# Optimization experiments

Measured on AMD Instinct MI355X. Metric: run time of the kernel, lower is better.

The kernel has to match this reference:

```python
import jax, jax.numpy as jnp
import numpy as np

MARGIN = 0.3


def _l2norm(x, axis=-1):
    return x / (jnp.linalg.norm(x, axis=axis, keepdims=True) + 1e-12)


def setup_inputs() -> dict:
    key = jax.random.key(0)
    k1, k2, k3, k4 = jax.random.split(key, 4)
    n, P, d = 1024, 8, 2048
    global_feat = jax.random.normal(k1, (n, d), dtype=jnp.float32)
    partial_feat = jax.random.normal(k2, (n, P, d), dtype=jnp.float32)
    part_labels = jax.random.randint(k3, (n, P), 0, 2).astype(jnp.float32)
    global_labels = jax.random.randint(k4, (n,), 0, 64).astype(jnp.int64)
    return {"global_feat": global_feat, "partial_feat": partial_feat,
            "part_labels": part_labels, "global_labels": global_labels}


def reference(global_feat, partial_feat, part_labels, global_labels):
    # --- compute_distance (VGTripletLoss) ---
    g = _l2norm(global_feat)            # [n, d]
    p = _l2norm(partial_feat)           # [n, P, d]
    gs = (1.0 - g @ g.T) / 2.0          # [n, n]
    overlap = part_labels[:, None, :] * part_labels[None, :, :]   # [n, n, P]
    # per-part cosine distance: [n, n, P]
    slf = (1.0 - jnp.einsum('ipd,jpd->ijp', p, p)) / 2.0
    slf = slf * overlap
    dist = (slf.sum(-1) + gs) / (overlap.sum(-1) + 1.0)            # [n, n]

    # --- compute_loss: hard positive/negative mining ---
    mask = global_labels[:, None] == global_labels[None, :]        # [n, n]
    neg_inf = jnp.float32(-1e30)
    pos_inf = jnp.float32(1e30)
    dist_ap = jnp.max(jnp.where(mask, dist, neg_inf), axis=1)      # hardest positive
    dist_an = jnp.min(jnp.where(mask, pos_inf, dist), axis=1)      # hardest negative
    # MarginRankingLoss(y=1, reduction='mean'): max(0, dist_ap - dist_an + margin)
    loss = jnp.mean(jax.nn.relu(dist_ap - dist_an + MARGIN))
    return loss
```

## Files before the change

### kernel.cpp

```cpp
#include <hip/hip_runtime.h>

#define N 1024
#define D 2048
#define P 8
#define F 9
#define KTOT (F * D)
#define BM 128
#define BKT 32
#define MARGIN 0.3f

typedef float f32x4 __attribute__((ext_vector_type(4)));
typedef short s16x8 __attribute__((ext_vector_type(8)));

#define GLOBAL_AS __attribute__((address_space(1)))
#define LDS_AS __attribute__((address_space(3)))

__device__ __forceinline__ const float* feat_row(const float* __restrict__ g,
                                                 const float* __restrict__ p,
                                                 int i, int f) {
    return (f == 0) ? (g + (size_t)i * D)
                    : (p + ((size_t)i * P + (f - 1)) * D);
}

__device__ __forceinline__ unsigned f2bf(float x) {
    unsigned u = __float_as_uint(x);
    return (u + 0x7fffu + ((u >> 16) & 1u)) >> 16;
}

__global__ __launch_bounds__(256)
void pack_kernel(const float* __restrict__ gfeat,
                 const float* __restrict__ pfeat,
                 const float* __restrict__ plab,
                 unsigned short* __restrict__ V) {
    const int wid = (blockIdx.x << 2) | (threadIdx.x >> 6);
    const int lane = threadIdx.x & 63;
    const int i = wid / F, f = wid % F;
    const float* src = feat_row(gfeat, pfeat, i, f);
    const float4* s4 = (const float4*)src;
    float4 a[4][2];
    #pragma unroll
    for (int q = 0; q < 4; ++q) {
        a[q][0] = s4[(q * 64 + lane) * 2];
        a[q][1] = s4[(q * 64 + lane) * 2 + 1];
    }
    float ss = 0.f;
    #pragma unroll
    for (int q = 0; q < 4; ++q)
        #pragma unroll
        for (int h = 0; h < 2; ++h)
            ss += a[q][h].x * a[q][h].x + a[q][h].y * a[q][h].y
                + a[q][h].z * a[q][h].z + a[q][h].w * a[q][h].w;
    #pragma unroll
    for (int m = 32; m > 0; m >>= 1) ss += __shfl_xor(ss, m, 64);
    const float ls = (f == 0) ? 1.0f : plab[i * P + (f - 1)];
    const float inv = ls / (sqrtf(ss) + 1e-12f);
    unsigned short* dst = V + (size_t)wid * D;
    #pragma unroll
    for (int q = 0; q < 4; ++q) {
        uint4 o;
        o.x = f2bf(a[q][0].x * inv) | (f2bf(a[q][0].y * inv) << 16);
        o.y = f2bf(a[q][0].z * inv) | (f2bf(a[q][0].w * inv) << 16);
        o.z = f2bf(a[q][1].x * inv) | (f2bf(a[q][1].y * inv) << 16);
        o.w = f2bf(a[q][1].z * inv) | (f2bf(a[q][1].w * inv) << 16);
        *(uint4*)&dst[(size_t)(q * 64 + lane) * 8] = o;
    }
}

__global__ __launch_bounds__(256)
void gemm_kernel(const unsigned short* __restrict__ V,
                 float* __restrict__ part, int ks) {
    __shared__ short As[2][BM * BKT];
    __shared__ short Bs[2][BM * BKT];

    const int nwg = gridDim.x * gridDim.y;
    const int l = blockIdx.x + gridDim.x * blockIdx.y;
    const int q = nwg >> 3;
    const int wg = (l & 7) * q + (l >> 3);
    const int t36 = wg % 36;
    const int bz = wg / 36;

    int by = 0, rem = t36;
    while (rem >= 8 - by) { rem -= 8 - by; ++by; }
    const int bx = by + rem;

    const int t = threadIdx.x;
    const int wave = t >> 6, lane = t & 63;
    const int i0 = by * BM;
    const int j0 = bx * BM;
    const int kbase = bz * ks;
    const int nsteps = ks >> 5;

    const int srow = t >> 2;
    const int schunk = (t & 3) ^ ((t >> 3) & 3);
    const unsigned short* Ag = V + (size_t)(i0 + srow) * KTOT + kbase + schunk * 8;
    const unsigned short* Bg = V + (size_t)(j0 + srow) * KTOT + kbase + schunk * 8;

    const int kq = lane >> 4;
    const int rsw = ((lane & 15) >> 1) & 3;
    const int kk = (kq ^ rsw) * 8;
    const int arow0 = (wave & 1) * 64 + (lane & 15);
    const int brow0 = (wave >> 1) * 64 + (lane & 15);

    f32x4 acc[4][4];
    #pragma unroll
    for (int m = 0; m < 4; ++m)
        #pragma unroll
        for (int n = 0; n < 4; ++n)
            acc[m][n] = (f32x4){0.f, 0.f, 0.f, 0.f};

#define STAGE(b) do {                                                          \
    __builtin_amdgcn_global_load_lds((const GLOBAL_AS void*)Ag,                \
        (LDS_AS void*)(&As[(b)][t * 8]), 16, 0, 0);                            \
    __builtin_amdgcn_global_load_lds((const GLOBAL_AS void*)(Ag + (size_t)64 * KTOT), \
        (LDS_AS void*)(&As[(b)][2048 + t * 8]), 16, 0, 0);                     \
    __builtin_amdgcn_global_load_lds((const GLOBAL_AS void*)Bg,                \
        (LDS_AS void*)(&Bs[(b)][t * 8]), 16, 0, 0);                            \
    __builtin_amdgcn_global_load_lds((const GLOBAL_AS void*)(Bg + (size_t)64 * KTOT), \
        (LDS_AS void*)(&Bs[(b)][2048 + t * 8]), 16, 0, 0);                     \
    Ag += BKT; Bg += BKT;                                                      \
} while (0)

#define COMPUTE(b) do {                                                        \
    s16x8 af[4], bf[4];                                                        \
    _Pragma("unroll")                                                          \
    for (int m = 0; m < 4; ++m)                                                \
        af[m] = *(const s16x8*)(&As[(b)][(arow0 + m * 16) * 32 + kk]);         \
    _Pragma("unroll")                                                          \
    for (int n = 0; n < 4; ++n)                                                \
        bf[n] = *(const s16x8*)(&Bs[(b)][(brow0 + n * 16) * 32 + kk]);         \
    _Pragma("unroll")                                                          \
    for (int m = 0; m < 4; ++m)                                                \
        _Pragma("unroll")                                                      \
        for (int n = 0; n < 4; ++n)                                            \
            acc[m][n] = __builtin_amdgcn_mfma_f32_16x16x32_bf16(               \
                af[m], bf[n], acc[m][n], 0, 0, 0);                             \
} while (0)

    STAGE(0);

    int cur = 0;
    for (int ksi = 0; ksi < nsteps - 1; ++ksi) {
        STAGE(cur ^ 1);
        asm volatile("s_waitcnt vmcnt(4)" ::: "memory");
        __builtin_amdgcn_s_barrier();
        COMPUTE(cur);
        __builtin_amdgcn_s_barrier();
        cur ^= 1;
    }
    asm volatile("s_waitcnt vmcnt(0)" ::: "memory");
    __builtin_amdgcn_s_barrier();
    COMPUTE(cur);

#undef STAGE
#undef COMPUTE

    float* outp = part + (size_t)bz * N * N;
    const int rbase = i0 + (wave & 1) * 64 + (lane >> 4) * 4;
    const int cbase = j0 + (wave >> 1) * 64 + (lane & 15);
    #pragma unroll
    for (int m = 0; m < 4; ++m)
        #pragma unroll
        for (int n = 0; n < 4; ++n)
            #pragma unroll
            for (int r = 0; r < 4; ++r)
                outp[(size_t)(rbase + m * 16 + r) * N + cbase + n * 16] = acc[m][n][r];

    if (bx != by) {
        #pragma unroll
        for (int m = 0; m < 4; ++m)
            #pragma unroll
            for (int n = 0; n < 4; ++n)
                #pragma unroll
                for (int r = 0; r < 4; ++r)
                    outp[(size_t)(cbase + n * 16) * N + rbase + m * 16 + r] = acc[m][n][r];
    }
}

template <int S>
__global__ __launch_bounds__(256)
void mine_kernel(const float* __restrict__ part,
                 const float* __restrict__ plab,
                 const int* __restrict__ glab,
                 float* __restrict__ rowloss) {
    const int i0 = blockIdx.x * 4;
    const int t = threadIdx.x;
    const int wave = t >> 6, lane = t & 63;
    const int j = t * 4;

    float labj[4][8];
    const float4* pj = (const float4*)&plab[(size_t)j * P];
    #pragma unroll
    for (int qq = 0; qq < 8; ++qq) ((float4*)labj)[qq] = pj[qq];
    const int4 gj = *(const int4*)&glab[j];
    const int gv[4] = {gj.x, gj.y, gj.z, gj.w};

    __shared__ float sap[4], san[4];

    #pragma unroll
    for (int ri = 0; ri < 4; ++ri) {
        const int i = i0 + ri;

        float4 dot = {0.f, 0.f, 0.f, 0.f};
        #pragma unroll
        for (int s = 0; s < S; ++s) {
            float4 v = *(const float4*)&part[(size_t)s * N * N + (size_t)i * N + j];
            dot.x += v.x; dot.y += v.y; dot.z += v.z; dot.w += v.w;
        }

        const int li = glab[i];
        float lab_i[P];
        #pragma unroll
        for (int c = 0; c < P; ++c) lab_i[c] = plab[i * P + c];

        float ap = -1e30f, an = 1e30f;
        const float dv[4] = {dot.x, dot.y, dot.z, dot.w};
        #pragma unroll
        for (int u = 0; u < 4; ++u) {
            float ov = 0.f;
            #pragma unroll
            for (int c = 0; c < P; ++c) ov += lab_i[c] * labj[u][c];
            float d = 0.5f - dv[u] / (2.0f * (ov + 1.0f));
            if (gv[u] == li) ap = fmaxf(ap, d);
            else             an = fminf(an, d);
        }

        #pragma unroll
        for (int m = 32; m > 0; m >>= 1) {
            ap = fmaxf(ap, __shfl_xor(ap, m, 64));
            an = fminf(an, __shfl_xor(an, m, 64));
        }
        if (lane == 0) { sap[wave] = ap; san[wave] = an; }
        __syncthreads();
        if (t == 0) {
            float A = fmaxf(fmaxf(sap[0], sap[1]), fmaxf(sap[2], sap[3]));
            float B = fminf(fminf(san[0], san[1]), fminf(san[2], san[3]));
            rowloss[i] = fmaxf(0.f, A - B + MARGIN);
        }
        __syncthreads();
    }
}

__global__ void reduce_kernel(const float* __restrict__ rowloss,
                              float* __restrict__ out) {
    const int t = threadIdx.x;
    float s = rowloss[t] + rowloss[t + 256] + rowloss[t + 512] + rowloss[t + 768];
    __shared__ float red[256];
    red[t] = s;
    __syncthreads();
    for (int st = 128; st > 0; st >>= 1) {
        if (t < st) red[t] += red[t + st];
        __syncthreads();
    }
    if (t == 0) out[0] = red[0] * (1.0f / N);
}

extern "C" void kernel_launch(void* const* d_in, const int* in_sizes, int n_in,
                              void* d_out, int out_size, void* d_ws, size_t ws_size,
                              hipStream_t stream) {
    const float* gfeat = (const float*)d_in[0];
    const float* pfeat = (const float*)d_in[1];
    const float* plab  = (const float*)d_in[2];
    const int*   glab  = (const int*)d_in[3];
    float* out = (float*)d_out;

    const size_t vbytes = (size_t)N * KTOT * 2;
    const size_t slice  = (size_t)N * N * 4;

    int S = (ws_size != 0 && ws_size >= vbytes + 16 * slice + 4096) ? 16 : 8;
    const int ks = KTOT / S;

    char* ws = (char*)d_ws;
    unsigned short* V = (unsigned short*)ws;
    float* part    = (float*)(ws + vbytes);
    float* rowloss = (float*)(ws + vbytes + (size_t)S * slice);

    pack_kernel<<<N * F / 4, 256, 0, stream>>>(gfeat, pfeat, plab, V);
    gemm_kernel<<<dim3(36, S), 256, 0, stream>>>(V, part, ks);
    if (S == 16)
        mine_kernel<16><<<N / 4, 256, 0, stream>>>(part, plab, glab, rowloss);
    else
        mine_kernel<8><<<N / 4, 256, 0, stream>>>(part, plab, glab, rowloss);
    reduce_kernel<<<1, 256, 0, stream>>>(rowloss, out);
}
```

Before: 164.1 us.

## Reduce split-K partial tiles with float atomics into one buffer

Split-K GEMM slices no longer write separate N×N partial buffers. They now atomically add into a single zeroed buffer, and the split count rises to 24. The mining kernel then reads one float4 per element instead of summing S slices, which removes most of the partial-buffer write and read traffic. The cost is atomic contention, an extra memset, and a summation order that is no longer deterministic.

```diff
diff --git a/kernel.cpp b/kernel.cpp
--- a/kernel.cpp
+++ b/kernel.cpp
@@ -7,6 +7,7 @@
 #define KTOT (F * D)
 #define BM 128
 #define BKT 32
+#define SPLIT 24
 #define MARGIN 0.3f
 
 typedef float f32x4 __attribute__((ext_vector_type(4)));
@@ -154,7 +155,6 @@
 #undef STAGE
 #undef COMPUTE
 
-    float* outp = part + (size_t)bz * N * N;
     const int rbase = i0 + (wave & 1) * 64 + (lane >> 4) * 4;
     const int cbase = j0 + (wave >> 1) * 64 + (lane & 15);
     #pragma unroll
@@ -163,7 +163,8 @@
         for (int n = 0; n < 4; ++n)
             #pragma unroll
             for (int r = 0; r < 4; ++r)
-                outp[(size_t)(rbase + m * 16 + r) * N + cbase + n * 16] = acc[m][n][r];
+                atomicAdd(&part[(size_t)(rbase + m * 16 + r) * N + cbase + n * 16],
+                          acc[m][n][r]);
 
     if (bx != by) {
         #pragma unroll
@@ -172,11 +173,11 @@
             for (int n = 0; n < 4; ++n)
                 #pragma unroll
                 for (int r = 0; r < 4; ++r)
-                    outp[(size_t)(cbase + n * 16) * N + rbase + m * 16 + r] = acc[m][n][r];
-    }
-}
-
-template <int S>
+                    atomicAdd(&part[(size_t)(cbase + n * 16) * N + rbase + m * 16 + r],
+                              acc[m][n][r]);
+    }
+}
+
 __global__ __launch_bounds__(256)
 void mine_kernel(const float* __restrict__ part,
                  const float* __restrict__ plab,
@@ -200,12 +201,7 @@
     for (int ri = 0; ri < 4; ++ri) {
         const int i = i0 + ri;
 
-        float4 dot = {0.f, 0.f, 0.f, 0.f};
-        #pragma unroll
-        for (int s = 0; s < S; ++s) {
-            float4 v = *(const float4*)&part[(size_t)s * N * N + (size_t)i * N + j];
-            dot.x += v.x; dot.y += v.y; dot.z += v.z; dot.w += v.w;
-        }
+        float4 dot = *(const float4*)&part[(size_t)i * N + j];
 
         const int li = glab[i];
         float lab_i[P];
@@ -264,21 +260,18 @@
     float* out = (float*)d_out;
 
     const size_t vbytes = (size_t)N * KTOT * 2;
-    const size_t slice  = (size_t)N * N * 4;
-
-    int S = (ws_size != 0 && ws_size >= vbytes + 16 * slice + 4096) ? 16 : 8;
-    const int ks = KTOT / S;
+    const size_t pbytes = (size_t)N * N * 4;
 
     char* ws = (char*)d_ws;
     unsigned short* V = (unsigned short*)ws;
     float* part    = (float*)(ws + vbytes);
-    float* rowloss = (float*)(ws + vbytes + (size_t)S * slice);
-
+    float* rowloss = (float*)(ws + vbytes + pbytes);
+
+    const int ks = KTOT / SPLIT;
+
+    hipMemsetAsync(part, 0, pbytes, stream);
     pack_kernel<<<N * F / 4, 256, 0, stream>>>(gfeat, pfeat, plab, V);
-    gemm_kernel<<<dim3(36, S), 256, 0, stream>>>(V, part, ks);
-    if (S == 16)
-        mine_kernel<16><<<N / 4, 256, 0, stream>>>(part, plab, glab, rowloss);
-    else
-        mine_kernel<8><<<N / 4, 256, 0, stream>>>(part, plab, glab, rowloss);
+    gemm_kernel<<<dim3(36, SPLIT), 256, 0, stream>>>(V, part, ks);
+    mine_kernel<<<N / 4, 256, 0, stream>>>(part, plab, glab, rowloss);
     reduce_kernel<<<1, 256, 0, stream>>>(rowloss, out);
 }
```

After: 318.7 us. +94.3%, slower.
